# Optimization experiments

Measured on AMD Instinct MI355X. Metric: run time of the kernel, lower is better.

## Reference

```python
import jax, jax.numpy as jnp
import numpy as np
import math

C_ATOM = 128
C_PAIR = 16
N_HEADS = 4
C_HEAD = C_ATOM // N_HEADS
N_ATOMS = 2048

def _layer_norm(x, w, b, eps=1e-5):
    mu = jnp.mean(x, axis=-1, keepdims=True)
    var = jnp.var(x, axis=-1, keepdims=True)
    return (x - mu) * jax.lax.rsqrt(var + eps) * w + b

def setup_inputs() -> dict:
    key = jax.random.key(0)
    ks = jax.random.split(key, 20)
    s = 0.02
    return {
        "ql": jax.random.normal(ks[0], (N_ATOMS, C_ATOM), jnp.float32),
        "cl": jax.random.normal(ks[1], (N_ATOMS, C_ATOM), jnp.float32),
        "plm": jax.random.normal(ks[2], (N_ATOMS, N_ATOMS, C_PAIR), jnp.float32),
        "beta_mask": jax.random.normal(ks[3], (N_ATOMS, N_ATOMS), jnp.float32),
        "norm_q_w": jnp.ones((C_ATOM,), jnp.float32),
        "norm_q_b": jnp.zeros((C_ATOM,), jnp.float32),
        "norm_pair_w": jnp.ones((C_PAIR,), jnp.float32),
        "norm_pair_b": jnp.zeros((C_PAIR,), jnp.float32),
        "Wq": jax.random.normal(ks[4], (C_ATOM, C_ATOM), jnp.float32) * s,
        "bq": jnp.zeros((C_ATOM,), jnp.float32),
        "Wk": jax.random.normal(ks[5], (C_ATOM, C_ATOM), jnp.float32) * s,
        "Wv": jax.random.normal(ks[6], (C_ATOM, C_ATOM), jnp.float32) * s,
        "Wpb": jax.random.normal(ks[7], (N_HEADS, C_PAIR), jnp.float32) * s,
        "Wg": jax.random.normal(ks[8], (C_ATOM, C_ATOM), jnp.float32) * s,
        "Wo": jax.random.normal(ks[9], (C_ATOM, C_ATOM), jnp.float32) * s,
        "t_ln_w": jnp.ones((C_ATOM,), jnp.float32),
        "t_ln_b": jnp.zeros((C_ATOM,), jnp.float32),
        "W1": jax.random.normal(ks[10], (4 * C_ATOM, C_ATOM), jnp.float32) * s,
        "b1": jnp.zeros((4 * C_ATOM,), jnp.float32),
        "W2": jax.random.normal(ks[11], (C_ATOM, 4 * C_ATOM), jnp.float32) * s,
        "b2": jnp.zeros((C_ATOM,), jnp.float32),
    }

def reference(ql, cl, plm, beta_mask, norm_q_w, norm_q_b, norm_pair_w, norm_pair_b,
              Wq, bq, Wk, Wv, Wpb, Wg, Wo, t_ln_w, t_ln_b, W1, b1, W2, b2):
    n = ql.shape[0]
    ql_norm = _layer_norm(ql, norm_q_w, norm_q_b)  # [N, C]
    q = (ql_norm @ Wq.T + bq).reshape(n, N_HEADS, C_HEAD)
    k = (ql_norm @ Wk.T).reshape(n, N_HEADS, C_HEAD)
    v = (ql_norm @ Wv.T).reshape(n, N_HEADS, C_HEAD)
    # pair-biased logits: [H, N, N]
    logits = jnp.einsum('ihc,jhc->hij', q, k) / math.sqrt(C_HEAD)
    pair_bias = _layer_norm(plm, norm_pair_w, norm_pair_b) @ Wpb.T  # [N, N, H]
    logits = logits + jnp.transpose(pair_bias, (2, 0, 1)) + beta_mask[None]
    attn = jax.nn.softmax(logits, axis=-1)
    attn_out = jnp.einsum('hij,jhc->ihc', attn, v).reshape(n, C_ATOM)
    gate = jax.nn.sigmoid(ql_norm @ Wg.T)
    out = (gate * attn_out) @ Wo.T
    ql = ql + out
    # transition MLP
    t = _layer_norm(ql, t_ln_w, t_ln_b)
    ql = ql + jax.nn.relu(t @ W1.T + b1) @ W2.T + b2
    return ql
```

## Files before the change

kernel.cpp:

```cpp
#include <hip/hip_runtime.h>
#include <hip/hip_bf16.h>
#include <math.h>

#define NA 2048
#define CP 16

__global__ __launch_bounds__(256) void bias_kernel(
    const float* __restrict__ plm, const float* __restrict__ beta_mask,
    const float* __restrict__ npw, const float* __restrict__ npb,
    const float* __restrict__ Wpb,
    __hip_bfloat16* __restrict__ biasT)
{
    const int t = threadIdx.x;
    const int i = blockIdx.x >> 2;
    const int j0 = (blockIdx.x & 3) * 512 + t * 2;

    float p[2][4];
#pragma unroll
    for (int e = 0; e < 2; ++e) {
        const size_t base = ((size_t)i * NA + (size_t)(j0 + e)) * CP;
        const float4 x0 = *(const float4*)(plm + base);
        const float4 x1 = *(const float4*)(plm + base + 4);
        const float4 x2 = *(const float4*)(plm + base + 8);
        const float4 x3 = *(const float4*)(plm + base + 12);
        float x[16] = {x0.x, x0.y, x0.z, x0.w, x1.x, x1.y, x1.z, x1.w,
                       x2.x, x2.y, x2.z, x2.w, x3.x, x3.y, x3.z, x3.w};
        float s = 0.f, s2 = 0.f;
#pragma unroll
        for (int c = 0; c < 16; ++c) {
            s += x[c];
            s2 = fmaf(x[c], x[c], s2);
        }
        const float mu = s * 0.0625f;
        const float inv = rsqrtf(s2 * 0.0625f - mu * mu + 1e-5f);
        float a0 = 0.f, a1 = 0.f, a2 = 0.f, a3 = 0.f;
#pragma unroll
        for (int c = 0; c < 16; ++c) {
            const float xn = (x[c] - mu) * inv * npw[c] + npb[c];
            a0 = fmaf(xn, Wpb[c], a0);
            a1 = fmaf(xn, Wpb[16 + c], a1);
            a2 = fmaf(xn, Wpb[32 + c], a2);
            a3 = fmaf(xn, Wpb[48 + c], a3);
        }
        p[e][0] = a0; p[e][1] = a1; p[e][2] = a2; p[e][3] = a3;
    }
    const float2 bm = *(const float2*)(beta_mask + (size_t)i * NA + j0);
#pragma unroll
    for (int h = 0; h < 4; ++h) {
        const __hip_bfloat162 o =
            __float22bfloat162_rn(make_float2(p[0][h] + bm.x, p[1][h] + bm.y));
        *(__hip_bfloat162*)(biasT + (size_t)h * NA * NA + (size_t)i * NA + j0) = o;
    }
}

__global__ __launch_bounds__(256) void qkvg_kernel(
    const float* __restrict__ ql,
    const float* __restrict__ nqw, const float* __restrict__ nqb,
    const float* __restrict__ Wq, const float* __restrict__ bq,
    const float* __restrict__ Wk, const float* __restrict__ Wv,
    const float* __restrict__ Wg,
    float* __restrict__ q_out, float* __restrict__ kT_out,
    float* __restrict__ vT_out, float* __restrict__ g_out)
{
    __shared__ float x_lds[4 * 128];
    __shared__ float xn_lds[4 * 128];
    const int t = threadIdx.x;
    const int row0 = blockIdx.x * 4;

    for (int idx = t; idx < 512; idx += 256)
        x_lds[idx] = ql[(size_t)row0 * 128 + idx];
    __syncthreads();

    if (t < 128) {
        const int r = t >> 5, id = t & 31;
        const float4 x4 = ((const float4*)x_lds)[r * 32 + id];
        float s = x4.x + x4.y + x4.z + x4.w;
        float s2 = x4.x * x4.x + x4.y * x4.y + x4.z * x4.z + x4.w * x4.w;
#pragma unroll
        for (int m = 16; m >= 1; m >>= 1) {
            s += __shfl_xor(s, m);
            s2 += __shfl_xor(s2, m);
        }
        const float mu = s * (1.0f / 128.0f);
        const float inv = rsqrtf(s2 * (1.0f / 128.0f) - mu * mu + 1e-5f);
#pragma unroll
        for (int k = 0; k < 4; ++k) {
            const int c = id * 4 + k;
            xn_lds[r * 128 + c] = (x_lds[r * 128 + c] - mu) * inv * nqw[c] + nqb[c];
        }
    }
    __syncthreads();

    const float4* xn4 = (const float4*)xn_lds;
#pragma unroll
    for (int cc = 0; cc < 2; ++cc) {
        const int col = cc * 256 + t;
        const int m = col >> 7;
        const int cl = col & 127;
        const float* W = (m == 0) ? Wq : (m == 1) ? Wk : (m == 2) ? Wv : Wg;
        float acc[4] = {0, 0, 0, 0};
        const float4* wrow = (const float4*)(W + (size_t)cl * 128);
#pragma unroll 8
        for (int k4 = 0; k4 < 32; ++k4) {
            const float4 w4 = wrow[k4];
#pragma unroll
            for (int r = 0; r < 4; ++r) {
                const float4 a = xn4[r * 32 + k4];
                acc[r] += a.x * w4.x + a.y * w4.y + a.z * w4.z + a.w * w4.w;
            }
        }
        if (m == 0) {
            const float bb = bq[cl];
            const float sc = 0.17677669529663687f;
#pragma unroll
            for (int r = 0; r < 4; ++r)
                q_out[(size_t)(row0 + r) * 128 + cl] = (acc[r] + bb) * sc;
        } else if (m == 1) {
            float4 o; o.x = acc[0]; o.y = acc[1]; o.z = acc[2]; o.w = acc[3];
            *(float4*)(kT_out + (size_t)cl * NA + row0) = o;
        } else if (m == 2) {
            float4 o; o.x = acc[0]; o.y = acc[1]; o.z = acc[2]; o.w = acc[3];
            *(float4*)(vT_out + (size_t)cl * NA + row0) = o;
        } else {
#pragma unroll
            for (int r = 0; r < 4; ++r)
                g_out[(size_t)(row0 + r) * 128 + cl] = 1.0f / (1.0f + __expf(-acc[r]));
        }
    }
}

__global__ __launch_bounds__(256) void attn_kernel(
    const __hip_bfloat16* __restrict__ biasT,
    const float* __restrict__ q_ws, const float* __restrict__ kT,
    const float* __restrict__ vT, const float* __restrict__ g_ws,
    float* __restrict__ attn_g)
{
    __shared__ unsigned short Lp[8][2048];
    __shared__ float q_s[8 * 32];
    __shared__ float redA[4 * 8];
    __shared__ float redB[4 * 8];

    const int t = threadIdx.x;
    const int h = blockIdx.x & 3;
    const int i0 = (blockIdx.x >> 2) * 8;
    const int w = t >> 6, lane = t & 63;
    const int jq = w * 512;

    q_s[t] = q_ws[(size_t)(i0 + (t >> 5)) * 128 + h * 32 + (t & 31)];
    __syncthreads();

    float4 La[8], Lb[8];
#pragma unroll
    for (int r = 0; r < 8; ++r) {
        const __hip_bfloat16* base = biasT + (size_t)h * NA * NA + (size_t)(i0 + r) * NA;
        const __hip_bfloat162* ba = (const __hip_bfloat162*)(base + jq + lane * 4);
        const float2 f0 = __bfloat1622float2(ba[0]);
        const float2 f1 = __bfloat1622float2(ba[1]);
        La[r] = make_float4(f0.x, f0.y, f1.x, f1.y);
        const __hip_bfloat162* bb = (const __hip_bfloat162*)(base + jq + 256 + lane * 4);
        const float2 g0 = __bfloat1622float2(bb[0]);
        const float2 g1 = __bfloat1622float2(bb[1]);
        Lb[r] = make_float4(g0.x, g0.y, g1.x, g1.y);
    }

    const float* kb = kT + (size_t)(h * 32) * NA + jq + lane * 4;
#pragma unroll 4
    for (int c = 0; c < 32; ++c) {
        const float4 ka = *(const float4*)(kb + (size_t)c * NA);
        const float4 kc = *(const float4*)(kb + (size_t)c * NA + 256);
#pragma unroll
        for (int r = 0; r < 8; ++r) {
            const float qv = q_s[r * 32 + c];
            La[r].x += qv * ka.x; La[r].y += qv * ka.y;
            La[r].z += qv * ka.z; La[r].w += qv * ka.w;
            Lb[r].x += qv * kc.x; Lb[r].y += qv * kc.y;
            Lb[r].z += qv * kc.z; Lb[r].w += qv * kc.w;
        }
    }

#pragma unroll
    for (int r = 0; r < 8; ++r) {
        float m = fmaxf(fmaxf(fmaxf(La[r].x, La[r].y), fmaxf(La[r].z, La[r].w)),
                        fmaxf(fmaxf(Lb[r].x, Lb[r].y), fmaxf(Lb[r].z, Lb[r].w)));
#pragma unroll
        for (int mk = 32; mk >= 1; mk >>= 1) m = fmaxf(m, __shfl_xor(m, mk));
        if (lane == 0) redA[w * 8 + r] = m;
    }
    __syncthreads();
#pragma unroll
    for (int r = 0; r < 8; ++r) {
        const float m = fmaxf(fmaxf(redA[r], redA[8 + r]), fmaxf(redA[16 + r], redA[24 + r]));
        La[r].x = __expf(La[r].x - m); La[r].y = __expf(La[r].y - m);
        La[r].z = __expf(La[r].z - m); La[r].w = __expf(La[r].w - m);
        Lb[r].x = __expf(Lb[r].x - m); Lb[r].y = __expf(Lb[r].y - m);
        Lb[r].z = __expf(Lb[r].z - m); Lb[r].w = __expf(Lb[r].w - m);
        float s = La[r].x + La[r].y + La[r].z + La[r].w +
                  Lb[r].x + Lb[r].y + Lb[r].z + Lb[r].w;
#pragma unroll
        for (int mk = 32; mk >= 1; mk >>= 1) s += __shfl_xor(s, mk);
        if (lane == 0) redB[w * 8 + r] = s;
    }
    __syncthreads();
#pragma unroll
    for (int r = 0; r < 8; ++r) {
        const float invl = 1.0f / (redB[r] + redB[8 + r] + redB[16 + r] + redB[24 + r]);
        __hip_bfloat162* d = (__hip_bfloat162*)&Lp[r][jq + lane * 4];
        d[0] = __float22bfloat162_rn(make_float2(La[r].x * invl, La[r].y * invl));
        d[1] = __float22bfloat162_rn(make_float2(La[r].z * invl, La[r].w * invl));
        __hip_bfloat162* d2 = (__hip_bfloat162*)&Lp[r][jq + 256 + lane * 4];
        d2[0] = __float22bfloat162_rn(make_float2(Lb[r].x * invl, Lb[r].y * invl));
        d2[1] = __float22bfloat162_rn(make_float2(Lb[r].z * invl, Lb[r].w * invl));
    }
    __syncthreads();

    float o[8][8];
#pragma unroll
    for (int r = 0; r < 8; ++r)
#pragma unroll
        for (int cc = 0; cc < 8; ++cc) o[r][cc] = 0.0f;

    const float* vb0 = vT + (size_t)(h * 32 + w * 8) * NA;
#pragma unroll 2
    for (int jf = 0; jf < 8; ++jf) {
        const int joff = jf * 256 + lane * 4;
        float2 pa[8], pb[8];
#pragma unroll
        for (int r = 0; r < 8; ++r) {
            const uint2 u = *(const uint2*)&Lp[r][joff];
            pa[r] = __bfloat1622float2(*(const __hip_bfloat162*)&u.x);
            pb[r] = __bfloat1622float2(*(const __hip_bfloat162*)&u.y);
        }
#pragma unroll
        for (int cc = 0; cc < 8; ++cc) {
            const float4 v4 = *(const float4*)(vb0 + (size_t)cc * NA + joff);
#pragma unroll
            for (int r = 0; r < 8; ++r) {
                o[r][cc] += pa[r].x * v4.x + pa[r].y * v4.y +
                            pb[r].x * v4.z + pb[r].y * v4.w;
            }
        }
    }

    __syncthreads();
    float* op = (float*)&Lp[0][0];
#pragma unroll
    for (int r = 0; r < 8; ++r) {
#pragma unroll
        for (int cc = 0; cc < 8; ++cc) {
            float s = o[r][cc];
            s += __shfl_xor(s, 32);
            s += __shfl_xor(s, 16);
            s += __shfl_xor(s, 8);
            o[r][cc] = s;
        }
    }
    if (lane < 8) {
#pragma unroll
        for (int r = 0; r < 8; ++r)
#pragma unroll
            for (int cc = 0; cc < 8; ++cc)
                op[((w * 8 + r) * 8 + cc) * 8 + lane] = o[r][cc];
    }
    __syncthreads();

    {
        const float4 a = ((const float4*)op)[t * 2];
        const float4 b = ((const float4*)op)[t * 2 + 1];
        const float s = a.x + a.y + a.z + a.w + b.x + b.y + b.z + b.w;
        const int r = (t >> 3) & 7;
        const int c = (t >> 6) * 8 + (t & 7);
        const float g = g_ws[(size_t)(i0 + r) * 128 + h * 32 + c];
        attn_g[(size_t)(i0 + r) * 128 + h * 32 + c] = s * g;
    }
}

__global__ __launch_bounds__(256) void out_mlp_kernel(
    const float* __restrict__ ql,
    const float* __restrict__ attn_g,
    const float* __restrict__ Wo,
    const float* __restrict__ tlw, const float* __restrict__ tlb,
    const float* __restrict__ W1, const float* __restrict__ b1,
    const float* __restrict__ W2, const float* __restrict__ b2,
    float* __restrict__ out)
{
    __shared__ float a_lds[4 * 128];
    __shared__ float ql2_lds[4 * 128];
    __shared__ float t_lds[4 * 128];
    __shared__ float h1_lds[4 * 512];
    const int t = threadIdx.x;
    const int row0 = blockIdx.x * 4;

    for (int idx = t; idx < 512; idx += 256)
        a_lds[idx] = attn_g[(size_t)row0 * 128 + idx];
    __syncthreads();

    {
        const int col = t >> 1, kh = t & 1;
        float p[4] = {0, 0, 0, 0};
        const float4* wr = (const float4*)(Wo + (size_t)col * 128 + kh * 64);
        const float4* a4 = (const float4*)a_lds;
#pragma unroll 8
        for (int k4 = 0; k4 < 16; ++k4) {
            const float4 w4 = wr[k4];
#pragma unroll
            for (int r = 0; r < 4; ++r) {
                const float4 a = a4[r * 32 + kh * 16 + k4];
                p[r] += a.x * w4.x + a.y * w4.y + a.z * w4.z + a.w * w4.w;
            }
        }
#pragma unroll
        for (int r = 0; r < 4; ++r) p[r] += __shfl_xor(p[r], 1);
        if (kh == 0) {
#pragma unroll
            for (int r = 0; r < 4; ++r)
                ql2_lds[r * 128 + col] = ql[(size_t)(row0 + r) * 128 + col] + p[r];
        }
    }
    __syncthreads();

    if (t < 128) {
        const int r = t >> 5, id = t & 31;
        const float4 x4 = ((const float4*)ql2_lds)[r * 32 + id];
        float s = x4.x + x4.y + x4.z + x4.w;
        float s2 = x4.x * x4.x + x4.y * x4.y + x4.z * x4.z + x4.w * x4.w;
#pragma unroll
        for (int m = 16; m >= 1; m >>= 1) {
            s += __shfl_xor(s, m);
            s2 += __shfl_xor(s2, m);
        }
        const float mu = s * (1.0f / 128.0f);
        const float inv = rsqrtf(s2 * (1.0f / 128.0f) - mu * mu + 1e-5f);
#pragma unroll
        for (int k = 0; k < 4; ++k) {
            const int c = id * 4 + k;
            t_lds[r * 128 + c] = (ql2_lds[r * 128 + c] - mu) * inv * tlw[c] + tlb[c];
        }
    }
    __syncthreads();

    const float4* t4 = (const float4*)t_lds;
#pragma unroll
    for (int cc = 0; cc < 2; ++cc) {
        const int col = cc * 256 + t;
        float acc[4] = {0, 0, 0, 0};
        const float4* wr = (const float4*)(W1 + (size_t)col * 128);
#pragma unroll 8
        for (int k4 = 0; k4 < 32; ++k4) {
            const float4 w4 = wr[k4];
#pragma unroll
            for (int r = 0; r < 4; ++r) {
                const float4 a = t4[r * 32 + k4];
                acc[r] += a.x * w4.x + a.y * w4.y + a.z * w4.z + a.w * w4.w;
            }
        }
        const float bb = b1[col];
#pragma unroll
        for (int r = 0; r < 4; ++r)
            h1_lds[r * 512 + col] = fmaxf(acc[r] + bb, 0.0f);
    }
    __syncthreads();

    {
        const int col = t >> 1, kh = t & 1;
        float p[4] = {0, 0, 0, 0};
        const float4* wr = (const float4*)(W2 + (size_t)col * 512 + kh * 256);
        const float4* h4 = (const float4*)h1_lds;
#pragma unroll 8
        for (int k4 = 0; k4 < 64; ++k4) {
            const float4 w4 = wr[k4];
#pragma unroll
            for (int r = 0; r < 4; ++r) {
                const float4 a = h4[r * 128 + kh * 64 + k4];
                p[r] += a.x * w4.x + a.y * w4.y + a.z * w4.z + a.w * w4.w;
            }
        }
#pragma unroll
        for (int r = 0; r < 4; ++r) p[r] += __shfl_xor(p[r], 1);
        if (kh == 0) {
            const float bb = b2[col];
#pragma unroll
            for (int r = 0; r < 4; ++r)
                out[(size_t)(row0 + r) * 128 + col] = ql2_lds[r * 128 + col] + p[r] + bb;
        }
    }
}

extern "C" void kernel_launch(void* const* d_in, const int* in_sizes, int n_in,
                              void* d_out, int out_size, void* d_ws, size_t ws_size,
                              hipStream_t stream) {
    const float* ql   = (const float*)d_in[0];
    const float* plm  = (const float*)d_in[2];
    const float* beta = (const float*)d_in[3];
    const float* nqw  = (const float*)d_in[4];
    const float* nqb  = (const float*)d_in[5];
    const float* npw  = (const float*)d_in[6];
    const float* npb  = (const float*)d_in[7];
    const float* Wq   = (const float*)d_in[8];
    const float* bq   = (const float*)d_in[9];
    const float* Wk   = (const float*)d_in[10];
    const float* Wv   = (const float*)d_in[11];
    const float* Wpb  = (const float*)d_in[12];
    const float* Wg   = (const float*)d_in[13];
    const float* Wo   = (const float*)d_in[14];
    const float* tlw  = (const float*)d_in[15];
    const float* tlb  = (const float*)d_in[16];
    const float* W1   = (const float*)d_in[17];
    const float* b1   = (const float*)d_in[18];
    const float* W2   = (const float*)d_in[19];
    const float* b2   = (const float*)d_in[20];
    float* out = (float*)d_out;

    char* ws = (char*)d_ws;
    __hip_bfloat16* biasT = (__hip_bfloat16*)ws;
    float* q_ws  = (float*)(ws + 33554432);
    float* g_ws  = (float*)(ws + 33554432 + 1 * 1048576);
    float* kT_ws = (float*)(ws + 33554432 + 2 * 1048576);
    float* vT_ws = (float*)(ws + 33554432 + 3 * 1048576);
    float* ag_ws = (float*)(ws + 33554432 + 4 * 1048576);

    bias_kernel<<<NA * 4, 256, 0, stream>>>(plm, beta, npw, npb, Wpb, biasT);
    qkvg_kernel<<<NA / 4, 256, 0, stream>>>(ql, nqw, nqb, Wq, bq, Wk, Wv, Wg,
                                            q_ws, kT_ws, vT_ws, g_ws);
    attn_kernel<<<NA / 2, 256, 0, stream>>>(biasT, q_ws, kT_ws, vT_ws, g_ws, ag_ws);
    out_mlp_kernel<<<NA / 4, 256, 0, stream>>>(ql, ag_ws, Wo, tlw, tlb,
                                               W1, b1, W2, b2, out);
}
```

Before: 523.3 us.

## Fuse four stages into one cooperative persistent kernel with grid syncs

Replaces four separate launches (pair bias, QKVG projection, attention, output MLP) with one cooperative kernel of 1024 blocks that runs each stage in turn, separated by grid-wide syncs. The work split per block changes: projection and MLP stages now handle 2 rows per block, and the attention stage handles 8 query rows of one head, keeping logits in registers and probabilities in LDS. The aim is to remove launch gaps and tail effects between kernels, at the cost of grid sync overhead and a forced occupancy of 4 blocks per CU. If the cooperative launch fails, it falls back to the original four kernels.

Result: slower. 1.505 ms (+187.6%).

```diff
diff --git a/kernel.cpp b/kernel.cpp
--- a/kernel.cpp
+++ b/kernel.cpp
@@ -1,9 +1,387 @@
 #include <hip/hip_runtime.h>
+#include <hip/hip_cooperative_groups.h>
 #include <hip/hip_bf16.h>
 #include <math.h>
 
 #define NA 2048
 #define CP 16
+
+namespace cg = cooperative_groups;
+
+struct FusedParams {
+    const float* ql; const float* plm; const float* beta;
+    const float* nqw; const float* nqb; const float* npw; const float* npb;
+    const float* Wq; const float* bq; const float* Wk; const float* Wv;
+    const float* Wpb; const float* Wg; const float* Wo;
+    const float* tlw; const float* tlb;
+    const float* W1; const float* b1; const float* W2; const float* b2;
+    float* out;
+    __hip_bfloat16* biasT;
+    float* q_ws; float* g_ws; float* kT_ws; float* vT_ws; float* ag_ws;
+};
+
+__global__ __launch_bounds__(256, 4) void fused_kernel(FusedParams P)
+{
+    __shared__ __align__(16) char smem[34048];
+    const int t = threadIdx.x;
+    cg::grid_group grid = cg::this_grid();
+
+    for (int vb = blockIdx.x; vb < NA * 4; vb += 1024) {
+        const int i = vb >> 2;
+        const int j0 = (vb & 3) * 512 + t * 2;
+        float p[2][4];
+#pragma unroll
+        for (int e = 0; e < 2; ++e) {
+            const size_t base = ((size_t)i * NA + (size_t)(j0 + e)) * CP;
+            const float4 x0 = *(const float4*)(P.plm + base);
+            const float4 x1 = *(const float4*)(P.plm + base + 4);
+            const float4 x2 = *(const float4*)(P.plm + base + 8);
+            const float4 x3 = *(const float4*)(P.plm + base + 12);
+            float x[16] = {x0.x, x0.y, x0.z, x0.w, x1.x, x1.y, x1.z, x1.w,
+                           x2.x, x2.y, x2.z, x2.w, x3.x, x3.y, x3.z, x3.w};
+            float s = 0.f, s2 = 0.f;
+#pragma unroll
+            for (int c = 0; c < 16; ++c) {
+                s += x[c];
+                s2 = fmaf(x[c], x[c], s2);
+            }
+            const float mu = s * 0.0625f;
+            const float inv = rsqrtf(s2 * 0.0625f - mu * mu + 1e-5f);
+            float a0 = 0.f, a1 = 0.f, a2 = 0.f, a3 = 0.f;
+#pragma unroll
+            for (int c = 0; c < 16; ++c) {
+                const float xn = (x[c] - mu) * inv * P.npw[c] + P.npb[c];
+                a0 = fmaf(xn, P.Wpb[c], a0);
+                a1 = fmaf(xn, P.Wpb[16 + c], a1);
+                a2 = fmaf(xn, P.Wpb[32 + c], a2);
+                a3 = fmaf(xn, P.Wpb[48 + c], a3);
+            }
+            p[e][0] = a0; p[e][1] = a1; p[e][2] = a2; p[e][3] = a3;
+        }
+        const float2 bm = *(const float2*)(P.beta + (size_t)i * NA + j0);
+#pragma unroll
+        for (int h = 0; h < 4; ++h) {
+            const __hip_bfloat162 o =
+                __float22bfloat162_rn(make_float2(p[0][h] + bm.x, p[1][h] + bm.y));
+            *(__hip_bfloat162*)(P.biasT + (size_t)h * NA * NA + (size_t)i * NA + j0) = o;
+        }
+    }
+
+    __threadfence();
+    grid.sync();
+
+    {
+        float* x_lds = (float*)smem;
+        float* xn_lds = (float*)(smem + 1024);
+        const int row0 = blockIdx.x * 2;
+
+        x_lds[t] = P.ql[(size_t)row0 * 128 + t];
+        __syncthreads();
+
+        if (t < 64) {
+            const int r = t >> 5, id = t & 31;
+            const float4 x4 = ((const float4*)x_lds)[r * 32 + id];
+            float s = x4.x + x4.y + x4.z + x4.w;
+            float s2 = x4.x * x4.x + x4.y * x4.y + x4.z * x4.z + x4.w * x4.w;
+#pragma unroll
+            for (int m = 16; m >= 1; m >>= 1) {
+                s += __shfl_xor(s, m);
+                s2 += __shfl_xor(s2, m);
+            }
+            const float mu = s * (1.0f / 128.0f);
+            const float inv = rsqrtf(s2 * (1.0f / 128.0f) - mu * mu + 1e-5f);
+#pragma unroll
+            for (int k = 0; k < 4; ++k) {
+                const int c = id * 4 + k;
+                xn_lds[r * 128 + c] = (x_lds[r * 128 + c] - mu) * inv * P.nqw[c] + P.nqb[c];
+            }
+        }
+        __syncthreads();
+
+        const float4* xn4 = (const float4*)xn_lds;
+#pragma unroll
+        for (int cc = 0; cc < 2; ++cc) {
+            const int col = cc * 256 + t;
+            const int m = col >> 7;
+            const int cl = col & 127;
+            const float* W = (m == 0) ? P.Wq : (m == 1) ? P.Wk : (m == 2) ? P.Wv : P.Wg;
+            float acc[2] = {0, 0};
+            const float4* wrow = (const float4*)(W + (size_t)cl * 128);
+#pragma unroll 8
+            for (int k4 = 0; k4 < 32; ++k4) {
+                const float4 w4 = wrow[k4];
+#pragma unroll
+                for (int r = 0; r < 2; ++r) {
+                    const float4 a = xn4[r * 32 + k4];
+                    acc[r] += a.x * w4.x + a.y * w4.y + a.z * w4.z + a.w * w4.w;
+                }
+            }
+            if (m == 0) {
+                const float bb = P.bq[cl];
+                const float sc = 0.17677669529663687f;
+#pragma unroll
+                for (int r = 0; r < 2; ++r)
+                    P.q_ws[(size_t)(row0 + r) * 128 + cl] = (acc[r] + bb) * sc;
+            } else if (m == 1) {
+                float2 o; o.x = acc[0]; o.y = acc[1];
+                *(float2*)(P.kT_ws + (size_t)cl * NA + row0) = o;
+            } else if (m == 2) {
+                float2 o; o.x = acc[0]; o.y = acc[1];
+                *(float2*)(P.vT_ws + (size_t)cl * NA + row0) = o;
+            } else {
+#pragma unroll
+                for (int r = 0; r < 2; ++r)
+                    P.g_ws[(size_t)(row0 + r) * 128 + cl] = 1.0f / (1.0f + __expf(-acc[r]));
+            }
+        }
+    }
+
+    __threadfence();
+    grid.sync();
+
+    {
+        unsigned short (*Lp)[2048] = reinterpret_cast<unsigned short (*)[2048]>(smem);
+        float* q_s = (float*)(smem + 32768);
+        float* redA = (float*)(smem + 33792);
+        float* redB = (float*)(smem + 33920);
+
+        const int h = blockIdx.x & 3;
+        const int i0 = (blockIdx.x >> 2) * 8;
+        const int w = t >> 6, lane = t & 63;
+        const int jq = w * 512;
+
+        q_s[t] = P.q_ws[(size_t)(i0 + (t >> 5)) * 128 + h * 32 + (t & 31)];
+        __syncthreads();
+
+        float4 La[8], Lb[8];
+#pragma unroll
+        for (int r = 0; r < 8; ++r) {
+            const __hip_bfloat16* base = P.biasT + (size_t)h * NA * NA + (size_t)(i0 + r) * NA;
+            const __hip_bfloat162* ba = (const __hip_bfloat162*)(base + jq + lane * 4);
+            const float2 f0 = __bfloat1622float2(ba[0]);
+            const float2 f1 = __bfloat1622float2(ba[1]);
+            La[r] = make_float4(f0.x, f0.y, f1.x, f1.y);
+            const __hip_bfloat162* bb = (const __hip_bfloat162*)(base + jq + 256 + lane * 4);
+            const float2 g0 = __bfloat1622float2(bb[0]);
+            const float2 g1 = __bfloat1622float2(bb[1]);
+            Lb[r] = make_float4(g0.x, g0.y, g1.x, g1.y);
+        }
+
+        const float* kb = P.kT_ws + (size_t)(h * 32) * NA + jq + lane * 4;
+#pragma unroll 4
+        for (int c = 0; c < 32; ++c) {
+            const float4 ka = *(const float4*)(kb + (size_t)c * NA);
+            const float4 kc = *(const float4*)(kb + (size_t)c * NA + 256);
+#pragma unroll
+            for (int r = 0; r < 8; ++r) {
+                const float qv = q_s[r * 32 + c];
+                La[r].x += qv * ka.x; La[r].y += qv * ka.y;
+                La[r].z += qv * ka.z; La[r].w += qv * ka.w;
+                Lb[r].x += qv * kc.x; Lb[r].y += qv * kc.y;
+                Lb[r].z += qv * kc.z; Lb[r].w += qv * kc.w;
+            }
+        }
+
+#pragma unroll
+        for (int r = 0; r < 8; ++r) {
+            float m = fmaxf(fmaxf(fmaxf(La[r].x, La[r].y), fmaxf(La[r].z, La[r].w)),
+                            fmaxf(fmaxf(Lb[r].x, Lb[r].y), fmaxf(Lb[r].z, Lb[r].w)));
+#pragma unroll
+            for (int mk = 32; mk >= 1; mk >>= 1) m = fmaxf(m, __shfl_xor(m, mk));
+            if (lane == 0) redA[w * 8 + r] = m;
+        }
+        __syncthreads();
+#pragma unroll
+        for (int r = 0; r < 8; ++r) {
+            const float m = fmaxf(fmaxf(redA[r], redA[8 + r]), fmaxf(redA[16 + r], redA[24 + r]));
+            La[r].x = __expf(La[r].x - m); La[r].y = __expf(La[r].y - m);
+            La[r].z = __expf(La[r].z - m); La[r].w = __expf(La[r].w - m);
+            Lb[r].x = __expf(Lb[r].x - m); Lb[r].y = __expf(Lb[r].y - m);
+            Lb[r].z = __expf(Lb[r].z - m); Lb[r].w = __expf(Lb[r].w - m);
+            float s = La[r].x + La[r].y + La[r].z + La[r].w +
+                      Lb[r].x + Lb[r].y + Lb[r].z + Lb[r].w;
+#pragma unroll
+            for (int mk = 32; mk >= 1; mk >>= 1) s += __shfl_xor(s, mk);
+            if (lane == 0) redB[w * 8 + r] = s;
+        }
+        __syncthreads();
+#pragma unroll
+        for (int r = 0; r < 8; ++r) {
+            const float invl = 1.0f / (redB[r] + redB[8 + r] + redB[16 + r] + redB[24 + r]);
+            __hip_bfloat162* d = (__hip_bfloat162*)&Lp[r][jq + lane * 4];
+            d[0] = __float22bfloat162_rn(make_float2(La[r].x * invl, La[r].y * invl));
+            d[1] = __float22bfloat162_rn(make_float2(La[r].z * invl, La[r].w * invl));
+            __hip_bfloat162* d2 = (__hip_bfloat162*)&Lp[r][jq + 256 + lane * 4];
+            d2[0] = __float22bfloat162_rn(make_float2(Lb[r].x * invl, Lb[r].y * invl));
+            d2[1] = __float22bfloat162_rn(make_float2(Lb[r].z * invl, Lb[r].w * invl));
+        }
+        __syncthreads();
+
+        float o[8][8];
+#pragma unroll
+        for (int r = 0; r < 8; ++r)
+#pragma unroll
+            for (int cc = 0; cc < 8; ++cc) o[r][cc] = 0.0f;
+
+        const float* vb0 = P.vT_ws + (size_t)(h * 32 + w * 8) * NA;
+#pragma unroll 2
+        for (int jf = 0; jf < 8; ++jf) {
+            const int joff = jf * 256 + lane * 4;
+            float2 pa[8], pb[8];
+#pragma unroll
+            for (int r = 0; r < 8; ++r) {
+                const uint2 u = *(const uint2*)&Lp[r][joff];
+                pa[r] = __bfloat1622float2(*(const __hip_bfloat162*)&u.x);
+                pb[r] = __bfloat1622float2(*(const __hip_bfloat162*)&u.y);
+            }
+#pragma unroll
+            for (int cc = 0; cc < 8; ++cc) {
+                const float4 v4 = *(const float4*)(vb0 + (size_t)cc * NA + joff);
+#pragma unroll
+                for (int r = 0; r < 8; ++r) {
+                    o[r][cc] += pa[r].x * v4.x + pa[r].y * v4.y +
+                                pb[r].x * v4.z + pb[r].y * v4.w;
+                }
+            }
+        }
+
+        __syncthreads();
+        float* op = (float*)smem;
+#pragma unroll
+        for (int r = 0; r < 8; ++r) {
+#pragma unroll
+            for (int cc = 0; cc < 8; ++cc) {
+                float s = o[r][cc];
+                s += __shfl_xor(s, 32);
+                s += __shfl_xor(s, 16);
+                s += __shfl_xor(s, 8);
+                o[r][cc] = s;
+            }
+        }
+        if (lane < 8) {
+#pragma unroll
+            for (int r = 0; r < 8; ++r)
+#pragma unroll
+                for (int cc = 0; cc < 8; ++cc)
+                    op[((w * 8 + r) * 8 + cc) * 8 + lane] = o[r][cc];
+        }
+        __syncthreads();
+
+        {
+            const float4 a = ((const float4*)op)[t * 2];
+            const float4 b = ((const float4*)op)[t * 2 + 1];
+            const float s = a.x + a.y + a.z + a.w + b.x + b.y + b.z + b.w;
+            const int r = (t >> 3) & 7;
+            const int c = (t >> 6) * 8 + (t & 7);
+            const float g = P.g_ws[(size_t)(i0 + r) * 128 + h * 32 + c];
+            P.ag_ws[(size_t)(i0 + r) * 128 + h * 32 + c] = s * g;
+        }
+    }
+
+    __threadfence();
+    grid.sync();
+
+    {
+        float* a_lds  = (float*)smem;
+        float* ql2_lds = (float*)(smem + 1024);
+        float* t_lds  = (float*)(smem + 2048);
+        float* h1_lds = (float*)(smem + 3072);
+        const int row0 = blockIdx.x * 2;
+
+        a_lds[t] = P.ag_ws[(size_t)row0 * 128 + t];
+        __syncthreads();
+
+        {
+            const int col = t >> 1, kh = t & 1;
+            float p[2] = {0, 0};
+            const float4* wr = (const float4*)(P.Wo + (size_t)col * 128 + kh * 64);
+            const float4* a4 = (const float4*)a_lds;
+#pragma unroll 8
+            for (int k4 = 0; k4 < 16; ++k4) {
+                const float4 w4 = wr[k4];
+#pragma unroll
+                for (int r = 0; r < 2; ++r) {
+                    const float4 a = a4[r * 32 + kh * 16 + k4];
+                    p[r] += a.x * w4.x + a.y * w4.y + a.z * w4.z + a.w * w4.w;
+                }
+            }
+#pragma unroll
+            for (int r = 0; r < 2; ++r) p[r] += __shfl_xor(p[r], 1);
+            if (kh == 0) {
+#pragma unroll
+                for (int r = 0; r < 2; ++r)
+                    ql2_lds[r * 128 + col] = P.ql[(size_t)(row0 + r) * 128 + col] + p[r];
+            }
+        }
+        __syncthreads();
+
+        if (t < 64) {
+            const int r = t >> 5, id = t & 31;
+            const float4 x4 = ((const float4*)ql2_lds)[r * 32 + id];
+            float s = x4.x + x4.y + x4.z + x4.w;
+            float s2 = x4.x * x4.x + x4.y * x4.y + x4.z * x4.z + x4.w * x4.w;
+#pragma unroll
+            for (int m = 16; m >= 1; m >>= 1) {
+                s += __shfl_xor(s, m);
+                s2 += __shfl_xor(s2, m);
+            }
+            const float mu = s * (1.0f / 128.0f);
+            const float inv = rsqrtf(s2 * (1.0f / 128.0f) - mu * mu + 1e-5f);
+#pragma unroll
+            for (int k = 0; k < 4; ++k) {
+                const int c = id * 4 + k;
+                t_lds[r * 128 + c] = (ql2_lds[r * 128 + c] - mu) * inv * P.tlw[c] + P.tlb[c];
+            }
+        }
+        __syncthreads();
+
+        const float4* t4 = (const float4*)t_lds;
+#pragma unroll
+        for (int cc = 0; cc < 2; ++cc) {
+            const int col = cc * 256 + t;
+            float acc[2] = {0, 0};
+            const float4* wr = (const float4*)(P.W1 + (size_t)col * 128);
+#pragma unroll 8
+            for (int k4 = 0; k4 < 32; ++k4) {
+                const float4 w4 = wr[k4];
+#pragma unroll
+                for (int r = 0; r < 2; ++r) {
+                    const float4 a = t4[r * 32 + k4];
+                    acc[r] += a.x * w4.x + a.y * w4.y + a.z * w4.z + a.w * w4.w;
+                }
+            }
+            const float bb = P.b1[col];
+#pragma unroll
+            for (int r = 0; r < 2; ++r)
+                h1_lds[r * 512 + col] = fmaxf(acc[r] + bb, 0.0f);
+        }
+        __syncthreads();
+
+        {
+            const int col = t >> 1, kh = t & 1;
+            float p[2] = {0, 0};
+            const float4* wr = (const float4*)(P.W2 + (size_t)col * 512 + kh * 256);
+            const float4* h4 = (const float4*)h1_lds;
+#pragma unroll 8
+            for (int k4 = 0; k4 < 64; ++k4) {
+                const float4 w4 = wr[k4];
+#pragma unroll
+                for (int r = 0; r < 2; ++r) {
+                    const float4 a = h4[r * 128 + kh * 64 + k4];
+                    p[r] += a.x * w4.x + a.y * w4.y + a.z * w4.z + a.w * w4.w;
+                }
+            }
+#pragma unroll
+            for (int r = 0; r < 2; ++r) p[r] += __shfl_xor(p[r], 1);
+            if (kh == 0) {
+                const float bb = P.b2[col];
+#pragma unroll
+                for (int r = 0; r < 2; ++r)
+                    P.out[(size_t)(row0 + r) * 128 + col] = ql2_lds[r * 128 + col] + p[r] + bb;
+            }
+        }
+    }
+}
 
 __global__ __launch_bounds__(256) void bias_kernel(
     const float* __restrict__ plm, const float* __restrict__ beta_mask,
@@ -27,10 +405,7 @@
                        x2.x, x2.y, x2.z, x2.w, x3.x, x3.y, x3.z, x3.w};
         float s = 0.f, s2 = 0.f;
 #pragma unroll
-        for (int c = 0; c < 16; ++c) {
-            s += x[c];
-            s2 = fmaf(x[c], x[c], s2);
-        }
+        for (int c = 0; c < 16; ++c) { s += x[c]; s2 = fmaf(x[c], x[c], s2); }
         const float mu = s * 0.0625f;
         const float inv = rsqrtf(s2 * 0.0625f - mu * mu + 1e-5f);
         float a0 = 0.f, a1 = 0.f, a2 = 0.f, a3 = 0.f;
@@ -77,10 +452,7 @@
         float s = x4.x + x4.y + x4.z + x4.w;
         float s2 = x4.x * x4.x + x4.y * x4.y + x4.z * x4.z + x4.w * x4.w;
 #pragma unroll
-        for (int m = 16; m >= 1; m >>= 1) {
-            s += __shfl_xor(s, m);
-            s2 += __shfl_xor(s2, m);
-        }
+        for (int m = 16; m >= 1; m >>= 1) { s += __shfl_xor(s, m); s2 += __shfl_xor(s2, m); }
         const float mu = s * (1.0f / 128.0f);
         const float inv = rsqrtf(s2 * (1.0f / 128.0f) - mu * mu + 1e-5f);
 #pragma unroll
@@ -324,10 +696,7 @@
         float s = x4.x + x4.y + x4.z + x4.w;
         float s2 = x4.x * x4.x + x4.y * x4.y + x4.z * x4.z + x4.w * x4.w;
 #pragma unroll
-        for (int m = 16; m >= 1; m >>= 1) {
-            s += __shfl_xor(s, m);
-            s2 += __shfl_xor(s2, m);
-        }
+        for (int m = 16; m >= 1; m >>= 1) { s += __shfl_xor(s, m); s2 += __shfl_xor(s2, m); }
         const float mu = s * (1.0f / 128.0f);
         const float inv = rsqrtf(s2 * (1.0f / 128.0f) - mu * mu + 1e-5f);
 #pragma unroll
@@ -418,10 +787,27 @@
     float* vT_ws = (float*)(ws + 33554432 + 3 * 1048576);
     float* ag_ws = (float*)(ws + 33554432 + 4 * 1048576);
 
-    bias_kernel<<<NA * 4, 256, 0, stream>>>(plm, beta, npw, npb, Wpb, biasT);
-    qkvg_kernel<<<NA / 4, 256, 0, stream>>>(ql, nqw, nqb, Wq, bq, Wk, Wv, Wg,
-                                            q_ws, kT_ws, vT_ws, g_ws);
-    attn_kernel<<<NA / 2, 256, 0, stream>>>(biasT, q_ws, kT_ws, vT_ws, g_ws, ag_ws);
-    out_mlp_kernel<<<NA / 4, 256, 0, stream>>>(ql, ag_ws, Wo, tlw, tlb,
-                                               W1, b1, W2, b2, out);
+    FusedParams P;
+    P.ql = ql; P.plm = plm; P.beta = beta;
+    P.nqw = nqw; P.nqb = nqb; P.npw = npw; P.npb = npb;
+    P.Wq = Wq; P.bq = bq; P.Wk = Wk; P.Wv = Wv; P.Wpb = Wpb;
+    P.Wg = Wg; P.Wo = Wo; P.tlw = tlw; P.tlb = tlb;
+    P.W1 = W1; P.b1 = b1; P.W2 = W2; P.b2 = b2;
+    P.out = out; P.biasT = biasT;
+    P.q_ws = q_ws; P.g_ws = g_ws; P.kT_ws = kT_ws; P.vT_ws = vT_ws; P.ag_ws = ag_ws;
+
+    void* args[] = {&P};
+    hipError_t err = hipLaunchCooperativeKernel(
+        reinterpret_cast<const void*>(&fused_kernel),
+        dim3(1024), dim3(256), args, 0, stream);
+
+    if (err != hipSuccess) {
+        (void)hipGetLastError();
+        bias_kernel<<<NA * 4, 256, 0, stream>>>(plm, beta, npw, npb, Wpb, biasT);
+        qkvg_kernel<<<NA / 4, 256, 0, stream>>>(ql, nqw, nqb, Wq, bq, Wk, Wv, Wg,
+                                                q_ws, kT_ws, vT_ws, g_ws);
+        attn_kernel<<<NA / 2, 256, 0, stream>>>(biasT, q_ws, kT_ws, vT_ws, g_ws, ag_ws);
+        out_mlp_kernel<<<NA / 4, 256, 0, stream>>>(ql, ag_ws, Wo, tlw, tlb,
+                                                   W1, b1, W2, b2, out);
+    }
 }
```
